# Performance work log

Measured on AMD Instinct MI355X. Metric: run time of the kernel, lower is better.

Reference implementation:

```python
import jax, jax.numpy as jnp
import numpy as np

K = 16  # kNN neighbors


def _knn(xb, k):
    # xb: [N, H] -> [N, k] nearest-neighbor indices (self excluded)
    sq = jnp.sum(xb * xb, axis=-1)
    d = sq[:, None] + sq[None, :] - 2.0 * (xb @ xb.T)  # squared distances [N, N]
    n = xb.shape[0]
    big = jnp.asarray(1e30, d.dtype)
    d = d + jnp.eye(n, dtype=d.dtype) * big  # mask self-loops
    _, idx = jax.lax.top_k(-d, k)
    return idx


def _edgeconv(h, W0, b0, W1, b1, k):
    # Dynamic kNN graph on current features + EdgeConv with 2-layer MLP, aggr='add'
    idx = jax.vmap(lambda xb: _knn(xb, k))(h)                 # [B, N, k]
    xj = jax.vmap(lambda xb, ib: xb[ib])(h, idx)              # [B, N, k, H] gather neighbors
    xi = jnp.broadcast_to(h[:, :, None, :], xj.shape)         # [B, N, k, H]
    m = jnp.concatenate([xi, xj - xi], axis=-1)               # [B, N, k, 2H]
    e = jax.nn.elu(m @ W0 + b0)
    e = jax.nn.elu(e @ W1 + b1)
    return jnp.sum(e, axis=2)                                 # 'add' aggregation over neighbors


def _forward(x, W_in0, b_in0, W_in1, b_in1, W_in2, b_in2,
             W_e0, b_e0, W_e1, b_e1,
             W_o0, b_o0, W_o1, b_o1, W_o2, b_o2):
    # input network (in_layers=3)
    h = jax.nn.elu(x @ W_in0 + b_in0)
    h = jax.nn.elu(h @ W_in1 + b_in1)
    h = jax.nn.elu(h @ W_in2 + b_in2)
    # agg_layers=2 blocks of dynamic-kNN EdgeConv
    for l in range(W_e0.shape[0]):
        h = _edgeconv(h, W_e0[l], b_e0[l], W_e1[l], b_e1[l], K)
    # global max pool over nodes of each graph (pool='max')
    g = jnp.max(h, axis=1)                                    # [B, H]
    # output network (out_layers=3)
    g = jax.nn.elu(g @ W_o0 + b_o0)
    g = jax.nn.elu(g @ W_o1 + b_o1)
    logits = g @ W_o2 + b_o2
    return jax.nn.log_softmax(logits, axis=1)


def setup_inputs() -> dict:
    key = jax.random.key(0)
    ks = jax.random.split(key, 8)
    B, N, F, H, C, A = 128, 512, 5, 64, 10, 2
    s = jnp.float32(0.1)

    def w(k, shape):
        return jax.random.normal(k, shape, jnp.float32) * s

    return {
        'x': jax.random.normal(ks[0], (B, N, F), jnp.float32),
        'W_in0': w(ks[1], (F, H)), 'b_in0': jnp.zeros((H,), jnp.float32),
        'W_in1': w(ks[2], (H, H)), 'b_in1': jnp.zeros((H,), jnp.float32),
        'W_in2': w(ks[3], (H, H)), 'b_in2': jnp.zeros((H,), jnp.float32),
        'W_e0': w(ks[4], (A, 2 * H, H)), 'b_e0': jnp.zeros((A, H), jnp.float32),
        'W_e1': w(ks[5], (A, H, H)), 'b_e1': jnp.zeros((A, H), jnp.float32),
        'W_o0': w(ks[6], (H, H)), 'b_o0': jnp.zeros((H,), jnp.float32),
        'W_o1': w(ks[7], (H, H)), 'b_o1': jnp.zeros((H,), jnp.float32),
        'W_o2': w(jax.random.fold_in(key, 99), (H, C)), 'b_o2': jnp.zeros((C,), jnp.float32),
    }


def reference(x, W_in0, b_in0, W_in1, b_in1, W_in2, b_in2,
              W_e0, b_e0, W_e1, b_e1,
              W_o0, b_o0, W_o1, b_o1, W_o2, b_o2):
    return _forward(x, W_in0, b_in0, W_in1, b_in1, W_in2, b_in2,
                    W_e0, b_e0, W_e1, b_e1,
                    W_o0, b_o0, W_o1, b_o1, W_o2, b_o2)
```

## Files before the change

### kernel.cpp

```cpp
#include <hip/hip_runtime.h>
#include <hip/hip_fp16.h>
#include <cmath>

typedef _Float16 f16;
typedef _Float16 f16x8 __attribute__((ext_vector_type(8)));
typedef float f32x4 __attribute__((ext_vector_type(4)));

#define B_ 128
#define N_ 512
#define H_ 64
#define K_ 16

__device__ __forceinline__ float elu_(float x) { return x > 0.f ? x : (__expf(x) - 1.f); }
__device__ __forceinline__ unsigned umin_(unsigned a, unsigned b) { return a < b ? a : b; }
__device__ __forceinline__ unsigned umax_(unsigned a, unsigned b) { return a > b ? a : b; }
__device__ __forceinline__ f32x4 mfma16(f16x8 a, f16x8 b, f32x4 c) {
    return __builtin_amdgcn_mfma_f32_16x16x32_f16(a, b, c, 0, 0, 0);
}
__device__ __forceinline__ f32x4 splat4(float v) { f32x4 r; r[0]=v; r[1]=v; r[2]=v; r[3]=v; return r; }
__device__ __forceinline__ unsigned mbcnt_(unsigned long long mask) {
    return __builtin_amdgcn_mbcnt_hi((unsigned)(mask >> 32),
           __builtin_amdgcn_mbcnt_lo((unsigned)mask, 0u));
}
__device__ __forceinline__ f16 hexp_(f16 x) {
    __half h = *(__half*)&x; h = hexp(h); return *(f16*)&h;
}
__device__ __forceinline__ f16x8 elu8h_(f16x8 x) {
    f16x8 z; f16x8 one;
    #pragma unroll
    for (int i = 0; i < 8; ++i) { z[i] = (f16)0.f; one[i] = (f16)1.f; }
    f16x8 mx = __builtin_elementwise_max(x, z);
    f16x8 mn = __builtin_elementwise_min(x, z);
    f16x8 e;
    #pragma unroll
    for (int i = 0; i < 8; ++i) e[i] = hexp_(mn[i]);
    return mx + e - one;
}
__device__ __forceinline__ unsigned wmax64_(unsigned v) {
    v = umax_(v, (unsigned)__builtin_amdgcn_update_dpp(0, (int)v, 0x111, 0xf, 0xf, true));
    v = umax_(v, (unsigned)__builtin_amdgcn_update_dpp(0, (int)v, 0x112, 0xf, 0xf, true));
    v = umax_(v, (unsigned)__builtin_amdgcn_update_dpp(0, (int)v, 0x114, 0xf, 0xf, true));
    v = umax_(v, (unsigned)__builtin_amdgcn_update_dpp(0, (int)v, 0x118, 0xf, 0xf, true));
    v = umax_(v, (unsigned)__builtin_amdgcn_update_dpp(0, (int)v, 0x142, 0xa, 0xf, true));
    v = umax_(v, (unsigned)__builtin_amdgcn_update_dpp(0, (int)v, 0x143, 0xc, 0xf, true));
    return (unsigned)__builtin_amdgcn_readlane((int)v, 63);
}
__device__ __forceinline__ float rsum16lo_(float x) {
    x += __int_as_float(__builtin_amdgcn_update_dpp(0, __float_as_int(x), 0x101, 0xf, 0xf, true));
    x += __int_as_float(__builtin_amdgcn_update_dpp(0, __float_as_int(x), 0x102, 0xf, 0xf, true));
    x += __int_as_float(__builtin_amdgcn_update_dpp(0, __float_as_int(x), 0x104, 0xf, 0xf, true));
    x += __int_as_float(__builtin_amdgcn_update_dpp(0, __float_as_int(x), 0x108, 0xf, 0xf, true));
    return x;
}

__global__ __launch_bounds__(256) void mlp_kernel(const float* __restrict__ x,
        const float* __restrict__ W0, const float* __restrict__ b0,
        const float* __restrict__ W1, const float* __restrict__ b1,
        const float* __restrict__ W2, const float* __restrict__ b2,
        const float* __restrict__ We0, const float* __restrict__ We1,
        f16* __restrict__ PW, f16* __restrict__ QW, f16* __restrict__ W1T,
        f16* __restrict__ hout, float* __restrict__ sqout)
{
    __shared__ f16 tile[4][16*72];
    __shared__ f16 w1t[64*80];
    __shared__ f16 w2t[64*80];
    const int tid = threadIdx.x;
    const int lane = tid & 63, wid = tid >> 6;
    const int m = lane & 15, q = lane >> 4;
    const int rowbase = blockIdx.x*64 + wid*16;
    f16* tw = tile[wid];

    if (blockIdx.x < 128 && tid < 64) {
        const int l = blockIdx.x >> 6, k = blockIdx.x & 63;
        const float* A  = We0 + l*8192;
        const float* B1 = We1 + l*4096;
        const float wa = A[k*64 + tid];
        const float wb = A[(k+64)*64 + tid];
        const float w1 = B1[k*64 + tid];
        PW [l*4096 + tid*64 + k] = (f16)(wa - wb);
        QW [l*4096 + tid*64 + k] = (f16)wb;
        W1T[l*4096 + tid*64 + k] = (f16)w1;
    }

    {
        const int k  = tid >> 2;
        const int n0 = (tid & 3) << 4;
        #pragma unroll
        for (int jj = 0; jj < 4; ++jj) {
            const float4 v1 = *(const float4*)(W1 + k*64 + n0 + jj*4);
            const float4 v2 = *(const float4*)(W2 + k*64 + n0 + jj*4);
            const int nb = n0 + jj*4;
            w1t[(nb+0)*80 + k] = (f16)v1.x; w1t[(nb+1)*80 + k] = (f16)v1.y;
            w1t[(nb+2)*80 + k] = (f16)v1.z; w1t[(nb+3)*80 + k] = (f16)v1.w;
            w2t[(nb+0)*80 + k] = (f16)v2.x; w2t[(nb+1)*80 + k] = (f16)v2.y;
            w2t[(nb+2)*80 + k] = (f16)v2.z; w2t[(nb+3)*80 + k] = (f16)v2.w;
        }
    }

    f16x8 af0, af1;
    {
        const float* xp = x + (size_t)(rowbase + m)*5;
        #pragma unroll
        for (int jj = 0; jj < 8; ++jj) { int k = q*8+jj; af0[jj] = (k < 5) ? (f16)xp[k] : (f16)0.f; }
    }
    f32x4 acc[4];
    #pragma unroll
    for (int t = 0; t < 4; ++t) {
        f16x8 bf;
        #pragma unroll
        for (int jj = 0; jj < 8; ++jj) { int k = q*8+jj; bf[jj] = (k < 5) ? (f16)W0[k*64 + t*16+m] : (f16)0.f; }
        acc[t] = splat4(b0[t*16+m]);
        acc[t] = mfma16(af0, bf, acc[t]);
    }
    #pragma unroll
    for (int t = 0; t < 4; ++t)
        #pragma unroll
        for (int r = 0; r < 4; ++r)
            tw[(q*4+r)*72 + t*16+m] = (f16)elu_(acc[t][r]);
    af0 = *(const f16x8*)(tw + m*72 + q*8);
    af1 = *(const f16x8*)(tw + m*72 + q*8 + 32);
    __syncthreads();

    #pragma unroll
    for (int t = 0; t < 4; ++t) {
        f16x8 bfa = *(const f16x8*)(w1t + (t*16+m)*80 + q*8);
        f16x8 bfb = *(const f16x8*)(w1t + (t*16+m)*80 + q*8 + 32);
        acc[t] = splat4(b1[t*16+m]);
        acc[t] = mfma16(af0, bfa, acc[t]);
        acc[t] = mfma16(af1, bfb, acc[t]);
    }
    #pragma unroll
    for (int t = 0; t < 4; ++t)
        #pragma unroll
        for (int r = 0; r < 4; ++r)
            tw[(q*4+r)*72 + t*16+m] = (f16)elu_(acc[t][r]);
    af0 = *(const f16x8*)(tw + m*72 + q*8);
    af1 = *(const f16x8*)(tw + m*72 + q*8 + 32);

    #pragma unroll
    for (int t = 0; t < 4; ++t) {
        f16x8 bfa = *(const f16x8*)(w2t + (t*16+m)*80 + q*8);
        f16x8 bfb = *(const f16x8*)(w2t + (t*16+m)*80 + q*8 + 32);
        acc[t] = splat4(b2[t*16+m]);
        acc[t] = mfma16(af0, bfa, acc[t]);
        acc[t] = mfma16(af1, bfb, acc[t]);
    }
    float s[4] = {0.f,0.f,0.f,0.f};
    #pragma unroll
    for (int t = 0; t < 4; ++t)
        #pragma unroll
        for (int r = 0; r < 4; ++r) {
            float v = elu_(acc[t][r]);
            hout[(size_t)(rowbase + q*4 + r)*64 + t*16 + m] = (f16)v;
            s[r] += v*v;
        }
    #pragma unroll
    for (int r = 0; r < 4; ++r) s[r] = rsum16lo_(s[r]);
    if (m == 0) {
        #pragma unroll
        for (int r = 0; r < 4; ++r) sqout[rowbase + q*4 + r] = s[r];
    }
}

__global__ __launch_bounds__(512, 8) void knn_kernel(const f16* __restrict__ hin,
        const float* __restrict__ sq, int* __restrict__ idxout,
        const f16* __restrict__ PWl, const float* __restrict__ be,
        const f16* __restrict__ QWl,
        f16* __restrict__ Pout, f16* __restrict__ Qout)
{
    __shared__ unsigned keys[16*512];
    const int lane = threadIdx.x & 63;
    const int wid  = threadIdx.x >> 6;
    const int m = lane & 15, q = lane >> 4;
    const int bid = ((blockIdx.x & 7) << 9) | (blockIdx.x >> 3);
    const int b  = bid >> 5;
    const int rt = bid & 31;
    const int rowbase = rt*16;
    const f16* hb = hin + (size_t)b*N_*H_;
    const float* sqb = sq + b*N_;

    f16x8 af0, af1;
    {
        const f16* Ap = hb + (size_t)(rowbase + m)*64 + q*8;
        af0 = *(const f16x8*)Ap;
        af1 = *(const f16x8*)(Ap + 32);
    }
    const int colb0 = wid*16;
    f16x8 bf0[4], bf1[4];
    float sc[4];
    #pragma unroll
    for (int cti = 0; cti < 4; ++cti) {
        const f16* Bp = hb + (size_t)(colb0 + cti*128 + m)*64 + q*8;
        bf0[cti] = *(const f16x8*)Bp;
        bf1[cti] = *(const f16x8*)(Bp + 32);
        sc[cti] = sqb[colb0 + cti*128 + m];
    }
    int base_r[4];
    #pragma unroll
    for (int r = 0; r < 4; ++r) {
        const int row = q*4 + r;
        base_r[r] = row*512 + ((colb0 + m) ^ (row << 1));
    }
    #pragma unroll
    for (int cti = 0; cti < 4; ++cti) {
        f32x4 acc = splat4(0.f);
        acc = mfma16(af0, bf0[cti], acc);
        acc = mfma16(af1, bf1[cti], acc);
        #pragma unroll
        for (int r = 0; r < 4; ++r) {
            float d = fmaf(-2.f, acc[r], sc[cti]);
            unsigned u = __float_as_uint(d);
            u ^= (0x80000000u | (unsigned)((int)u >> 31));
            unsigned key = (u & 0xFFFFFE00u) | (unsigned)(colb0 + cti*128 + m);
            keys[base_r[r] + cti*128] = key;
        }
    }
    __syncthreads();

    unsigned kk[2][8];
    #pragma unroll
    for (int rr = 0; rr < 2; ++rr) {
        const int ri = wid*2 + rr;
        *(uint4*)&kk[rr][0] = *(const uint4*)(keys + ri*512 + lane*4);
        *(uint4*)&kk[rr][4] = *(const uint4*)(keys + ri*512 + 256 + lane*4);
    }
    unsigned* scr = keys + wid*2*512;

    unsigned v[2];
    #pragma unroll
    for (int rr = 0; rr < 2; ++rr) {
        unsigned mn = kk[rr][0];
        #pragma unroll
        for (int s2 = 1; s2 < 8; ++s2) mn = umin_(mn, kk[rr][s2]);
        v[rr] = mn;
    }
    unsigned T[2] = {0u,0u};
    #pragma unroll
    for (int bit = 31; bit >= 9; --bit) {
        #pragma unroll
        for (int rr = 0; rr < 2; ++rr) {
            unsigned cand = T[rr] | (1u << bit);
            int c = __popcll(__ballot(v[rr] < cand));
            T[rr] = (c < 17) ? cand : T[rr];
        }
    }
    T[0] |= 511u; T[1] |= 511u;

    unsigned cnt[2];
    #pragma unroll
    for (int rr = 0; rr < 2; ++rr) {
        unsigned long long bal[8];
        #pragma unroll
        for (int s2 = 0; s2 < 8; ++s2) bal[s2] = __ballot(kk[rr][s2] <= T[rr]);
        unsigned base = 0;
        #pragma unroll
        for (int s2 = 0; s2 < 8; ++s2) {
            if (kk[rr][s2] <= T[rr]) {
                unsigned pos = base + mbcnt_(bal[s2]);
                if (pos < 64u) scr[rr*64 + pos] = kk[rr][s2];
            }
            base += (unsigned)__popcll(bal[s2]);
        }
        cnt[rr] = base;
    }

    #pragma unroll
    for (int rr = 0; rr < 2; ++rr) {
        const unsigned cc_ = umin_(cnt[rr], 64u);
        const int ri = wid*2 + rr;
        const unsigned rowglob = (unsigned)(rowbase + ri);
        bool act = lane < (int)cc_;
        unsigned mv = act ? scr[rr*64 + lane] : 0u;
        if (act && (mv & 511u) == rowglob) { act = false; mv = 0u; }
        int e = __popcll(__ballot(act)) - 16;
        while (e > 0) {
            unsigned mx = wmax64_(mv);
            if (mv == mx) { act = false; mv = 0u; }
            --e;
        }
        int* outp = idxout + ((size_t)b*N_ + rowglob)*K_;
        unsigned long long bal = __ballot(act);
        unsigned rank = mbcnt_(bal);
        if (act) outp[rank] = (int)(mv & 511u);
    }

    {
        const int t = wid & 3;
        const int n = t*16 + m;
        f32x4 acc = (wid < 4) ? splat4(be[n]) : splat4(0.f);
        const f16* Wp = (wid < 4) ? PWl : QWl;
        #pragma unroll
        for (int cc = 0; cc < 2; ++cc) {
            const f16x8 afc = cc ? af1 : af0;
            const f16x8 bb = *(const f16x8*)(Wp + n*64 + cc*32 + q*8);
            acc = mfma16(afc, bb, acc);
        }
        f16* outp = (wid < 4) ? Pout : Qout;
        #pragma unroll
        for (int r = 0; r < 4; ++r)
            outp[((size_t)b*N_ + rowbase + q*4 + r)*64 + t*16 + m] = (f16)acc[r];
    }
}

__device__ __forceinline__ void edge_node_(size_t r0, f16x8 pa, f16x8 pb,
        f16x8 qa, f16x8 qb, const f16x8 (&bf)[2][4], const float (&bcol)[4],
        f16* __restrict__ out, float* __restrict__ sqout, int lane)
{
    f16x8 af0 = elu8h_(pa + qa);
    f16x8 af1 = elu8h_(pb + qb);
    f32x4 acc[4];
    #pragma unroll
    for (int t = 0; t < 4; ++t) acc[t] = splat4(bcol[t]);
    #pragma unroll
    for (int t = 0; t < 4; ++t) acc[t] = mfma16(af0, bf[0][t], acc[t]);
    #pragma unroll
    for (int t = 0; t < 4; ++t) acc[t] = mfma16(af1, bf[1][t], acc[t]);
    float ssum = 0.f;
    #pragma unroll
    for (int t = 0; t < 4; ++t) {
        float s = elu_(acc[t][0]) + elu_(acc[t][1]) + elu_(acc[t][2]) + elu_(acc[t][3]);
        s += __shfl_xor(s, 16);
        s += __shfl_xor(s, 32);
        if (lane < 16) out[r0*64 + t*16 + lane] = (f16)s;
        ssum += s*s;
    }
    ssum = rsum16lo_(ssum);
    if (lane == 0) sqout[r0] = ssum;
}

__global__ __launch_bounds__(256, 4) void edge_kernel(const f16* __restrict__ P,
        const f16* __restrict__ Q, const int* __restrict__ idx,
        const f16* __restrict__ W1T, const float* __restrict__ b1,
        f16* __restrict__ out, float* __restrict__ sqout)
{
    const int lane = threadIdx.x & 63;
    const int wid  = threadIdx.x >> 6;
    const int m = lane & 15, q = lane >> 4;

    f16x8 bf[2][4];
    #pragma unroll
    for (int cc = 0; cc < 2; ++cc)
        #pragma unroll
        for (int t = 0; t < 4; ++t)
            bf[cc][t] = *(const f16x8*)(W1T + (t*16 + m)*64 + cc*32 + q*8);
    float bcol[4];
    #pragma unroll
    for (int t = 0; t < 4; ++t) bcol[t] = b1[t*16 + m];

    const int bid = ((blockIdx.x & 7) << 10) | (blockIdx.x >> 3);
    const int node0 = bid*8 + wid*2;
    const int gbase = node0 & ~(N_-1);
    const int c0a = q*8, c0b = q*8 + 32;
    int jv[2];
    #pragma unroll
    for (int i = 0; i < 2; ++i) jv[i] = idx[(size_t)(node0 + i)*K_ + m];

    f16x8 pA[2], pB[2], qA[2], qB[2];
    #pragma unroll
    for (int k2 = 0; k2 < 2; ++k2) {
        const size_t r0 = (size_t)(node0 + k2);
        const size_t g0 = (size_t)(gbase + jv[k2]);
        pA[k2] = *(const f16x8*)(P + r0*64 + c0a);
        pB[k2] = *(const f16x8*)(P + r0*64 + c0b);
        qA[k2] = *(const f16x8*)(Q + g0*64 + c0a);
        qB[k2] = *(const f16x8*)(Q + g0*64 + c0b);
    }
    #pragma unroll
    for (int k2 = 0; k2 < 2; ++k2)
        edge_node_((size_t)(node0 + k2), pA[k2], pB[k2], qA[k2], qB[k2],
                   bf, bcol, out, sqout, lane);
}

__global__ __launch_bounds__(512) void final_kernel(const f16* __restrict__ hin,
        const float* __restrict__ Wo0, const float* __restrict__ bo0,
        const float* __restrict__ Wo1, const float* __restrict__ bo1,
        const float* __restrict__ Wo2, const float* __restrict__ bo2,
        float* __restrict__ out)
{
    __shared__ float smax[64][64];
    __shared__ float g0[64], g1[64], g2[64], part[8][64], lg[10];
    const int t = threadIdx.x;
    const int b = blockIdx.x;
    const int cg = t & 7, rg = t >> 3;

    float mx[8];
    #pragma unroll
    for (int e = 0; e < 8; ++e) mx[e] = -3.0e38f;
    #pragma unroll
    for (int i = 0; i < 8; ++i) {
        const int row = rg + i*64;
        f16x8 vv = *(const f16x8*)(hin + ((size_t)b*N_ + row)*64 + cg*8);
        #pragma unroll
        for (int e = 0; e < 8; ++e) mx[e] = fmaxf(mx[e], (float)vv[e]);
    }
    #pragma unroll
    for (int e = 0; e < 8; ++e) smax[rg][cg*8 + e] = mx[e];
    __syncthreads();
    for (int s = 32; s >= 1; s >>= 1) {
        if (rg < s) {
            #pragma unroll
            for (int e = 0; e < 8; ++e)
                smax[rg][cg*8+e] = fmaxf(smax[rg][cg*8+e], smax[rg+s][cg*8+e]);
        }
        __syncthreads();
    }
    if (t < 64) g0[t] = smax[0][t];
    __syncthreads();

    const int j = t & 63, p = t >> 6;
    {
        float a = 0.f;
        #pragma unroll
        for (int c = 0; c < 8; ++c) a += g0[p*8 + c]*Wo0[(p*8 + c)*64 + j];
        part[p][j] = a;
    }
    __syncthreads();
    if (t < 64) {
        float a = bo0[t];
        #pragma unroll
        for (int p2 = 0; p2 < 8; ++p2) a += part[p2][t];
        g1[t] = elu_(a);
    }
    __syncthreads();
    {
        float a = 0.f;
        #pragma unroll
        for (int c = 0; c < 8; ++c) a += g1[p*8 + c]*Wo1[(p*8 + c)*64 + j];
        part[p][j] = a;
    }
    __syncthreads();
    if (t < 64) {
        float a = bo1[t];
        #pragma unroll
        for (int p2 = 0; p2 < 8; ++p2) a += part[p2][t];
        g2[t] = elu_(a);
    }
    __syncthreads();
    if (t < 10) { float a = bo2[t]; for (int c = 0; c < 64; ++c) a += g2[c]*Wo2[c*10 + t]; lg[t] = a; }
    __syncthreads();
    if (t == 0) {
        float mxl = lg[0];
        for (int i = 1; i < 10; ++i) mxl = fmaxf(mxl, lg[i]);
        float s = 0.f;
        for (int i = 0; i < 10; ++i) s += expf(lg[i] - mxl);
        const float lse = mxl + logf(s);
        for (int i = 0; i < 10; ++i) out[b*10 + i] = lg[i] - lse;
    }
}

extern "C" void kernel_launch(void* const* d_in, const int* in_sizes, int n_in,
                              void* d_out, int out_size, void* d_ws, size_t ws_size,
                              hipStream_t stream) {
    const float* x     = (const float*)d_in[0];
    const float* W_in0 = (const float*)d_in[1];
    const float* b_in0 = (const float*)d_in[2];
    const float* W_in1 = (const float*)d_in[3];
    const float* b_in1 = (const float*)d_in[4];
    const float* W_in2 = (const float*)d_in[5];
    const float* b_in2 = (const float*)d_in[6];
    const float* W_e0  = (const float*)d_in[7];
    const float* b_e0  = (const float*)d_in[8];
    const float* W_e1  = (const float*)d_in[9];
    const float* b_e1  = (const float*)d_in[10];
    const float* Wo0   = (const float*)d_in[11];
    const float* bo0   = (const float*)d_in[12];
    const float* Wo1   = (const float*)d_in[13];
    const float* bo1   = (const float*)d_in[14];
    const float* Wo2   = (const float*)d_in[15];
    const float* bo2   = (const float*)d_in[16];

    char* ws = (char*)d_ws;
    f16*    hA   = (f16*)(ws);
    f16*    hB   = (f16*)(ws + 8388608);
    f16*    Pb   = (f16*)(ws + 16777216);
    f16*    Qb   = (f16*)(ws + 25165824);
    int*    idxb = (int*)(ws + 33554432);
    float*  sqb  = (float*)(ws + 37748736);
    f16*    PW   = (f16*)(ws + 38010880);
    f16*    QW   = (f16*)(ws + 38027264);
    f16*    W1T  = (f16*)(ws + 38043648);

    mlp_kernel<<<1024, 256, 0, stream>>>(x, W_in0, b_in0, W_in1, b_in1, W_in2, b_in2,
                                         W_e0, W_e1, PW, QW, W1T, hA, sqb);
    knn_kernel<<<4096, 512, 0, stream>>>(hA, sqb, idxb, PW, b_e0, QW, Pb, Qb);
    edge_kernel<<<8192, 256, 0, stream>>>(Pb, Qb, idxb, W1T, b_e1, hB, sqb);
    knn_kernel<<<4096, 512, 0, stream>>>(hB, sqb, idxb, PW + 4096, b_e0 + 64, QW + 4096, Pb, Qb);
    edge_kernel<<<8192, 256, 0, stream>>>(Pb, Qb, idxb, W1T + 4096, b_e1 + 64, hA, sqb);

    final_kernel<<<128, 512, 0, stream>>>(hA, Wo0, bo0, Wo1, bo1, Wo2, bo2, (float*)d_out);
}
```

Measured before the change: 315.5 us.

## Fuse global max-pool and output MLP into last edge kernel via atomics

```diff
diff --git a/kernel.cpp b/kernel.cpp
--- a/kernel.cpp
+++ b/kernel.cpp
@@ -52,6 +52,14 @@
     x += __int_as_float(__builtin_amdgcn_update_dpp(0, __float_as_int(x), 0x108, 0xf, 0xf, true));
     return x;
 }
+__device__ __forceinline__ unsigned fmap_(float f) {
+    int i = __float_as_int(f);
+    return (unsigned)(i ^ ((i >> 31) | 0x80000000));
+}
+__device__ __forceinline__ float funmap_(unsigned u) {
+    int i = (u & 0x80000000u) ? (int)(u ^ 0x80000000u) : (int)~u;
+    return __int_as_float(i);
+}
 
 __global__ __launch_bounds__(256) void mlp_kernel(const float* __restrict__ x,
         const float* __restrict__ W0, const float* __restrict__ b0,
@@ -59,6 +67,7 @@
         const float* __restrict__ W2, const float* __restrict__ b2,
         const float* __restrict__ We0, const float* __restrict__ We1,
         f16* __restrict__ PW, f16* __restrict__ QW, f16* __restrict__ W1T,
+        unsigned* __restrict__ maxbuf, unsigned* __restrict__ cntbuf,
         f16* __restrict__ hout, float* __restrict__ sqout)
 {
     __shared__ f16 tile[4][16*72];
@@ -80,6 +89,10 @@
         PW [l*4096 + tid*64 + k] = (f16)(wa - wb);
         QW [l*4096 + tid*64 + k] = (f16)wb;
         W1T[l*4096 + tid*64 + k] = (f16)w1;
+    } else if (blockIdx.x >= 128 && blockIdx.x < 256) {
+        const int batch = blockIdx.x - 128;
+        if (tid < 64) maxbuf[batch*64 + tid] = 0u;
+        else if (tid == 64) cntbuf[batch] = 0u;
     }
 
     {
@@ -302,9 +315,11 @@
     }
 }
 
+template<int LAST>
 __device__ __forceinline__ void edge_node_(size_t r0, f16x8 pa, f16x8 pb,
         f16x8 qa, f16x8 qb, const f16x8 (&bf)[2][4], const float (&bcol)[4],
-        f16* __restrict__ out, float* __restrict__ sqout, int lane)
+        f16* __restrict__ out, float* __restrict__ sqout, int lane,
+        float (&mxv)[4])
 {
     f16x8 af0 = elu8h_(pa + qa);
     f16x8 af1 = elu8h_(pb + qb);
@@ -321,20 +336,37 @@
         float s = elu_(acc[t][0]) + elu_(acc[t][1]) + elu_(acc[t][2]) + elu_(acc[t][3]);
         s += __shfl_xor(s, 16);
         s += __shfl_xor(s, 32);
-        if (lane < 16) out[r0*64 + t*16 + lane] = (f16)s;
-        ssum += s*s;
-    }
-    ssum = rsum16lo_(ssum);
-    if (lane == 0) sqout[r0] = ssum;
-}
-
+        if (LAST) {
+            mxv[t] = fmaxf(mxv[t], (float)(f16)s);
+        } else {
+            if (lane < 16) out[r0*64 + t*16 + lane] = (f16)s;
+            ssum += s*s;
+        }
+    }
+    if (!LAST) {
+        ssum = rsum16lo_(ssum);
+        if (lane == 0) sqout[r0] = ssum;
+    }
+}
+
+template<int LAST>
 __global__ __launch_bounds__(256, 4) void edge_kernel(const f16* __restrict__ P,
         const f16* __restrict__ Q, const int* __restrict__ idx,
         const f16* __restrict__ W1T, const float* __restrict__ b1,
-        f16* __restrict__ out, float* __restrict__ sqout)
+        f16* __restrict__ out, float* __restrict__ sqout,
+        unsigned* __restrict__ maxbuf, unsigned* __restrict__ cntbuf,
+        const float* __restrict__ Wo0, const float* __restrict__ bo0,
+        const float* __restrict__ Wo1, const float* __restrict__ bo1,
+        const float* __restrict__ Wo2, const float* __restrict__ bo2,
+        float* __restrict__ out10)
 {
-    const int lane = threadIdx.x & 63;
-    const int wid  = threadIdx.x >> 6;
+    __shared__ float lred[4][64];
+    __shared__ float gv[64];
+    __shared__ float lg[10];
+    __shared__ int lastflag;
+    const int tid  = threadIdx.x;
+    const int lane = tid & 63;
+    const int wid  = tid >> 6;
     const int m = lane & 15, q = lane >> 4;
 
     f16x8 bf[2][4];
@@ -347,17 +379,17 @@
     #pragma unroll
     for (int t = 0; t < 4; ++t) bcol[t] = b1[t*16 + m];
 
-    const int bid = ((blockIdx.x & 7) << 10) | (blockIdx.x >> 3);
-    const int node0 = bid*8 + wid*2;
+    const int bid = ((blockIdx.x & 7) << 9) | (blockIdx.x >> 3);
+    const int node0 = bid*16 + wid*4;
     const int gbase = node0 & ~(N_-1);
     const int c0a = q*8, c0b = q*8 + 32;
-    int jv[2];
-    #pragma unroll
-    for (int i = 0; i < 2; ++i) jv[i] = idx[(size_t)(node0 + i)*K_ + m];
-
-    f16x8 pA[2], pB[2], qA[2], qB[2];
-    #pragma unroll
-    for (int k2 = 0; k2 < 2; ++k2) {
+    int jv[4];
+    #pragma unroll
+    for (int i = 0; i < 4; ++i) jv[i] = idx[(size_t)(node0 + i)*K_ + m];
+
+    f16x8 pA[4], pB[4], qA[4], qB[4];
+    #pragma unroll
+    for (int k2 = 0; k2 < 4; ++k2) {
         const size_t r0 = (size_t)(node0 + k2);
         const size_t g0 = (size_t)(gbase + jv[k2]);
         pA[k2] = *(const f16x8*)(P + r0*64 + c0a);
@@ -365,86 +397,80 @@
         qA[k2] = *(const f16x8*)(Q + g0*64 + c0a);
         qB[k2] = *(const f16x8*)(Q + g0*64 + c0b);
     }
-    #pragma unroll
-    for (int k2 = 0; k2 < 2; ++k2)
-        edge_node_((size_t)(node0 + k2), pA[k2], pB[k2], qA[k2], qB[k2],
-                   bf, bcol, out, sqout, lane);
-}
-
-__global__ __launch_bounds__(512) void final_kernel(const f16* __restrict__ hin,
-        const float* __restrict__ Wo0, const float* __restrict__ bo0,
-        const float* __restrict__ Wo1, const float* __restrict__ bo1,
-        const float* __restrict__ Wo2, const float* __restrict__ bo2,
-        float* __restrict__ out)
-{
-    __shared__ float smax[64][64];
-    __shared__ float g0[64], g1[64], g2[64], part[8][64], lg[10];
-    const int t = threadIdx.x;
-    const int b = blockIdx.x;
-    const int cg = t & 7, rg = t >> 3;
-
-    float mx[8];
-    #pragma unroll
-    for (int e = 0; e < 8; ++e) mx[e] = -3.0e38f;
-    #pragma unroll
-    for (int i = 0; i < 8; ++i) {
-        const int row = rg + i*64;
-        f16x8 vv = *(const f16x8*)(hin + ((size_t)b*N_ + row)*64 + cg*8);
-        #pragma unroll
-        for (int e = 0; e < 8; ++e) mx[e] = fmaxf(mx[e], (float)vv[e]);
-    }
-    #pragma unroll
-    for (int e = 0; e < 8; ++e) smax[rg][cg*8 + e] = mx[e];
-    __syncthreads();
-    for (int s = 32; s >= 1; s >>= 1) {
-        if (rg < s) {
-            #pragma unroll
-            for (int e = 0; e < 8; ++e)
-                smax[rg][cg*8+e] = fmaxf(smax[rg][cg*8+e], smax[rg+s][cg*8+e]);
-        }
-        __syncthreads();
-    }
-    if (t < 64) g0[t] = smax[0][t];
-    __syncthreads();
-
-    const int j = t & 63, p = t >> 6;
+    float mxv[4] = {-3.0e38f, -3.0e38f, -3.0e38f, -3.0e38f};
+    #pragma unroll
+    for (int k2 = 0; k2 < 4; ++k2)
+        edge_node_<LAST>((size_t)(node0 + k2), pA[k2], pB[k2], qA[k2], qB[k2],
+                         bf, bcol, out, sqout, lane, mxv);
+
+    if (!LAST) return;
+
+    const int bglob = (bid*16) >> 9;
+    if (lane < 16) {
+        #pragma unroll
+        for (int t = 0; t < 4; ++t) lred[wid][t*16 + lane] = mxv[t];
+    }
+    __syncthreads();
+    if (tid < 64) {
+        float mm = fmaxf(fmaxf(lred[0][tid], lred[1][tid]),
+                         fmaxf(lred[2][tid], lred[3][tid]));
+        __hip_atomic_fetch_max(&maxbuf[bglob*64 + tid], fmap_(mm),
+                               __ATOMIC_RELEASE, __HIP_MEMORY_SCOPE_AGENT);
+    }
+    __syncthreads();
+    if (tid == 0) {
+        unsigned old = __hip_atomic_fetch_add(&cntbuf[bglob], 1u,
+                               __ATOMIC_ACQ_REL, __HIP_MEMORY_SCOPE_AGENT);
+        lastflag = (old == 31u);
+    }
+    __syncthreads();
+    if (!lastflag) return;
+
+    if (tid < 64) {
+        unsigned u = __hip_atomic_load(&maxbuf[bglob*64 + tid],
+                               __ATOMIC_ACQUIRE, __HIP_MEMORY_SCOPE_AGENT);
+        gv[tid] = funmap_(u);
+    }
+    __syncthreads();
+    const int j = tid & 63, p = tid >> 6;
     {
         float a = 0.f;
         #pragma unroll
-        for (int c = 0; c < 8; ++c) a += g0[p*8 + c]*Wo0[(p*8 + c)*64 + j];
-        part[p][j] = a;
-    }
-    __syncthreads();
-    if (t < 64) {
-        float a = bo0[t];
-        #pragma unroll
-        for (int p2 = 0; p2 < 8; ++p2) a += part[p2][t];
-        g1[t] = elu_(a);
+        for (int c = 0; c < 16; ++c) a += gv[p*16 + c] * Wo0[(p*16 + c)*64 + j];
+        lred[p][j] = a;
+    }
+    __syncthreads();
+    if (tid < 64) {
+        float a = bo0[tid] + lred[0][tid] + lred[1][tid] + lred[2][tid] + lred[3][tid];
+        gv[tid] = elu_(a);
     }
     __syncthreads();
     {
         float a = 0.f;
         #pragma unroll
-        for (int c = 0; c < 8; ++c) a += g1[p*8 + c]*Wo1[(p*8 + c)*64 + j];
-        part[p][j] = a;
-    }
-    __syncthreads();
-    if (t < 64) {
-        float a = bo1[t];
-        #pragma unroll
-        for (int p2 = 0; p2 < 8; ++p2) a += part[p2][t];
-        g2[t] = elu_(a);
-    }
-    __syncthreads();
-    if (t < 10) { float a = bo2[t]; for (int c = 0; c < 64; ++c) a += g2[c]*Wo2[c*10 + t]; lg[t] = a; }
-    __syncthreads();
-    if (t == 0) {
+        for (int c = 0; c < 16; ++c) a += gv[p*16 + c] * Wo1[(p*16 + c)*64 + j];
+        lred[p][j] = a;
+    }
+    __syncthreads();
+    if (tid < 64) {
+        float a = bo1[tid] + lred[0][tid] + lred[1][tid] + lred[2][tid] + lred[3][tid];
+        gv[tid] = elu_(a);
+    }
+    __syncthreads();
+    if (tid < 10) {
+        float a = bo2[tid];
+        #pragma unroll
+        for (int c = 0; c < 64; ++c) a += gv[c]*Wo2[c*10 + tid];
+        lg[tid] = a;
+    }
+    __syncthreads();
+    if (tid == 0) {
         float mxl = lg[0];
         for (int i = 1; i < 10; ++i) mxl = fmaxf(mxl, lg[i]);
         float s = 0.f;
         for (int i = 0; i < 10; ++i) s += expf(lg[i] - mxl);
         const float lse = mxl + logf(s);
-        for (int i = 0; i < 10; ++i) out[b*10 + i] = lg[i] - lse;
+        for (int i = 0; i < 10; ++i) out10[bglob*10 + i] = lg[i] - lse;
     }
 }
 
@@ -470,22 +496,26 @@
     const float* bo2   = (const float*)d_in[16];
 
     char* ws = (char*)d_ws;
-    f16*    hA   = (f16*)(ws);
-    f16*    hB   = (f16*)(ws + 8388608);
-    f16*    Pb   = (f16*)(ws + 16777216);
-    f16*    Qb   = (f16*)(ws + 25165824);
-    int*    idxb = (int*)(ws + 33554432);
-    float*  sqb  = (float*)(ws + 37748736);
-    f16*    PW   = (f16*)(ws + 38010880);
-    f16*    QW   = (f16*)(ws + 38027264);
-    f16*    W1T  = (f16*)(ws + 38043648);
+    f16*      hA   = (f16*)(ws);
+    f16*      hB   = (f16*)(ws + 8388608);
+    f16*      Pb   = (f16*)(ws + 16777216);
+    f16*      Qb   = (f16*)(ws + 25165824);
+    int*      idxb = (int*)(ws + 33554432);
+    float*    sqb  = (float*)(ws + 37748736);
+    f16*      PW   = (f16*)(ws + 38010880);
+    f16*      QW   = (f16*)(ws + 38027264);
+    f16*      W1T  = (f16*)(ws + 38043648);
+    unsigned* mxb  = (unsigned*)(ws + 38060032);
+    unsigned* cntb = (unsigned*)(ws + 38092800);
 
     mlp_kernel<<<1024, 256, 0, stream>>>(x, W_in0, b_in0, W_in1, b_in1, W_in2, b_in2,
-                                         W_e0, W_e1, PW, QW, W1T, hA, sqb);
+                                         W_e0, W_e1, PW, QW, W1T, mxb, cntb, hA, sqb);
     knn_kernel<<<4096, 512, 0, stream>>>(hA, sqb, idxb, PW, b_e0, QW, Pb, Qb);
-    edge_kernel<<<8192, 256, 0, stream>>>(Pb, Qb, idxb, W1T, b_e1, hB, sqb);
+    edge_kernel<0><<<4096, 256, 0, stream>>>(Pb, Qb, idxb, W1T, b_e1, hB, sqb,
+                                             nullptr, nullptr, nullptr, nullptr,
+                                             nullptr, nullptr, nullptr, nullptr, nullptr);
     knn_kernel<<<4096, 512, 0, stream>>>(hB, sqb, idxb, PW + 4096, b_e0 + 64, QW + 4096, Pb, Qb);
-    edge_kernel<<<8192, 256, 0, stream>>>(Pb, Qb, idxb, W1T + 4096, b_e1 + 64, hA, sqb);
-
-    final_kernel<<<128, 512, 0, stream>>>(hA, Wo0, bo0, Wo1, bo1, Wo2, bo2, (float*)d_out);
-}
+    edge_kernel<1><<<4096, 256, 0, stream>>>(Pb, Qb, idxb, W1T + 4096, b_e1 + 64, hA, sqb,
+                                             mxb, cntb, Wo0, bo0, Wo1, bo1, Wo2, bo2,
+                                             (float*)d_out);
+}
```

Result: slower. 420.0 us (+33.1%).
